# Performance work log

Hardware: AMD Instinct MI355X
Metric: run time of the kernel (lower is better)

Reference implementation:

```python
import jax, jax.numpy as jnp
import numpy as np

B, N_SPINS, D_MODEL, K_MC = 256, 128, 768, 25


def setup_inputs() -> dict:
    key = jax.random.key(0)
    k1, k2, k3 = jax.random.split(key, 3)
    features = jax.random.normal(k1, (B, N_SPINS, D_MODEL), dtype=jnp.float32)
    coalitions = jax.random.randint(k2, (K_MC, N_SPINS), 0, 2, dtype=jnp.int32)
    w_v = jax.random.normal(k3, (D_MODEL, D_MODEL), dtype=jnp.float32) * 0.02
    scale = jnp.full((1,), 0.1, dtype=jnp.float32)
    return {"features": features, "coalitions": coalitions, "w_v": w_v, "scale": scale}


def reference(features, coalitions, w_v, scale):
    # features: [B, n, d]; coalitions: [K, n] in {0,1}; w_v: [d, d]; scale: [1]
    c = coalitions.astype(features.dtype)                      # [K, n]
    # coalition_value batched over all K coalitions at once:
    # sum_j mask[k,j] * features[b,j,:]  (sum and linear proj commute)
    s = jnp.einsum('kn,bnd->bkd', c, features)                 # [B, K, d]
    proj = s @ w_v                                             # [B, K, d]
    norm = jnp.linalg.norm(proj, axis=-1)                      # [B, K]
    cv = jax.nn.relu(norm * scale[0])                          # coalition values [B, K]
    # Shapley estimate: mean(v | i in S) - mean(v | i not in S)
    cnt_with = c.sum(axis=0)                                   # [n]
    cnt_without = c.shape[0] - cnt_with
    v_with = (cv @ c) / jnp.maximum(cnt_with, 1.0)             # [B, n]
    v_without = (cv @ (1.0 - c)) / jnp.maximum(cnt_without, 1.0)
    valid = (cnt_with > 0) & (cnt_without > 0)                 # [n]
    shapley = jnp.where(valid, v_with - v_without, 0.0)        # [B, n]
    return shapley
```

## Files before the change

kernel.cpp:

```cpp
#include <hip/hip_runtime.h>
#include <hip/hip_bf16.h>
#include <stdint.h>

#define NB  256
#define NSP 128
#define DM  768
#define KMC 25
#define MROWS (NB*KMC)

#define OFF_S    0u
#define OFF_WT   9830400u
#define OFF_N2   11010048u
#define OFF_COEF 11035648u
#define OFF_CB   11049984u

typedef __attribute__((ext_vector_type(8))) short bf16x8;
typedef __attribute__((ext_vector_type(4))) float f32x4;
typedef unsigned int u32;

#define GLOAD_LDS16(gp, lp) \
  __builtin_amdgcn_global_load_lds((const __attribute__((address_space(1))) u32*)(gp), \
                                   (__attribute__((address_space(3))) u32*)(lp), 16, 0, 0)

__global__ __launch_bounds__(256) void prep_kernel(const float* __restrict__ wv,
                                                   const int* __restrict__ co,
                                                   char* __restrict__ ws) {
  const int blk = blockIdx.x;
  const int t = threadIdx.x;
  if (blk < 144) {
    __shared__ __hip_bfloat16 lt[64][66];
    const int bi = blk / 12, bj = blk % 12;
    const int k0 = bi * 64, n0 = bj * 64;
    #pragma unroll
    for (int i = 0; i < 16; ++i) {
      int idx = t + i * 256;
      int r = idx >> 6, c = idx & 63;
      lt[c][r] = __float2bfloat16(wv[(size_t)(k0 + r) * DM + n0 + c]);
    }
    __syncthreads();
    __hip_bfloat16* wT = (__hip_bfloat16*)(ws + OFF_WT);
    #pragma unroll
    for (int i = 0; i < 16; ++i) {
      int idx = t + i * 256;
      int r = idx >> 6, c = idx & 63;
      wT[(size_t)(n0 + r) * DM + k0 + c] = lt[r][c];
    }
  } else if (blk == 144) {
    if (t < NSP) {
      const int n = t;
      int cw = 0;
      for (int k = 0; k < KMC; ++k) cw += co[k * NSP + n];
      const int cwo = KMC - cw;
      const bool valid = (cw > 0) && (cwo > 0);
      float* coefT = (float*)(ws + OFF_COEF);
      for (int k = 0; k < 28; ++k) {
        float v = 0.f;
        if (valid && k < KMC) v = co[k * NSP + n] ? (1.f / (float)cw) : (-1.f / (float)cwo);
        coefT[n * 28 + k] = v;
      }
    }
  } else if (blk < 170) {
    int i = (blk - 145) * 256 + t;
    if (i < MROWS) ((float*)(ws + OFF_N2))[i] = 0.f;
  } else {
    __hip_bfloat16* Cb = (__hip_bfloat16*)(ws + OFF_CB);
    for (int i = t; i < 32 * NSP; i += 256) {
      int k = i >> 7, n = i & 127;
      float v = (k < KMC) ? (float)co[k * NSP + n] : 0.f;
      Cb[i] = __float2bfloat16(v);
    }
  }
}

__global__ __launch_bounds__(256) void kA(const float* __restrict__ f,
                                          const __hip_bfloat16* __restrict__ Cb,
                                          __hip_bfloat16* __restrict__ s) {
  const int b = blockIdx.x;
  const int half = blockIdx.y;
  const int tid = threadIdx.x;
  const int w = tid >> 6;
  const int lane = tid & 63;
  const int lo = lane & 15, hi = lane >> 4;

  bf16x8 A0[4], A1[4];
  #pragma unroll
  for (int ks = 0; ks < 4; ++ks) {
    A0[ks] = *(const bf16x8*)(Cb + (size_t)lo * NSP + ks * 32 + hi * 8);
    A1[ks] = *(const bf16x8*)(Cb + (size_t)(16 + lo) * NSP + ks * 32 + hi * 8);
  }

  const int dbase = half * 384 + w * 96;
  const float* fb = f + (size_t)b * NSP * DM + dbase + lo;

#define LOADT(dt, buf) { \
    const float* p_ = fb + (dt) * 16; \
    _Pragma("unroll") for (int ks = 0; ks < 4; ++ks) \
      _Pragma("unroll") for (int j = 0; j < 8; ++j) \
        buf[ks * 8 + j] = p_[(size_t)(ks * 32 + hi * 8 + j) * DM]; }

#define COMPUTE(dt, buf) { \
    bf16x8 Bf[4]; \
    _Pragma("unroll") for (int ks = 0; ks < 4; ++ks) \
      _Pragma("unroll") for (int j = 0; j < 8; ++j) { \
        __hip_bfloat16 h_ = __float2bfloat16(buf[ks * 8 + j]); \
        Bf[ks][j] = *(short*)&h_; } \
    f32x4 ac0 = {0.f, 0.f, 0.f, 0.f}, ac1 = {0.f, 0.f, 0.f, 0.f}; \
    _Pragma("unroll") for (int ks = 0; ks < 4; ++ks) { \
      ac0 = __builtin_amdgcn_mfma_f32_16x16x32_bf16(A0[ks], Bf[ks], ac0, 0, 0, 0); \
      ac1 = __builtin_amdgcn_mfma_f32_16x16x32_bf16(A1[ks], Bf[ks], ac1, 0, 0, 0); } \
    _Pragma("unroll") for (int i = 0; i < 4; ++i) { \
      int r0_ = hi * 4 + i; \
      s[((size_t)(b * KMC) + r0_) * DM + dbase + (dt) * 16 + lo] = __float2bfloat16(ac0[i]); \
      int r1_ = 16 + hi * 4 + i; \
      if (r1_ < KMC) \
        s[((size_t)(b * KMC) + r1_) * DM + dbase + (dt) * 16 + lo] = __float2bfloat16(ac1[i]); } }

  float bufA[32], bufB[32];
  LOADT(0, bufA)
  #pragma unroll
  for (int dt = 0; dt < 6; dt += 2) {
    if (dt + 1 < 6) LOADT(dt + 1, bufB)
    COMPUTE(dt, bufA)
    if (dt + 2 < 6) LOADT(dt + 2, bufA)
    if (dt + 1 < 6) COMPUTE(dt + 1, bufB)
  }
#undef LOADT
#undef COMPUTE
}

#define BM 128
#define BN 192
#define BK 32
#define NTK 24

__global__ __launch_bounds__(256) void kB(char* __restrict__ ws) {
  const int bid = blockIdx.x;
  const int tm = bid >> 2;
  const int tn = bid & 3;
  const int tid = threadIdx.x;
  const int wid = tid >> 6;
  const int lane = tid & 63;
  const int wm = wid >> 1;
  const int wn = wid & 1;

  const __hip_bfloat16* S  = (const __hip_bfloat16*)(ws + OFF_S);
  const __hip_bfloat16* WT = (const __hip_bfloat16*)(ws + OFF_WT);
  float* norm2 = (float*)(ws + OFF_N2);

  __shared__ __align__(16) char As[2][BM * BK * 2];
  __shared__ __align__(16) char Bs[2][BN * BK * 2];

  const char* gA[2]; char *lA0[2], *lA1[2];
  #pragma unroll
  for (int j = 0; j < 2; ++j) {
    int li = (wid * 2 + j) * 64 + lane;
    int r = li >> 2, sl = li & 3;
    int slx = sl ^ ((r >> 1) & 3);
    gA[j] = (const char*)(S + (size_t)(tm * BM + r) * DM) + slx * 16;
    lA0[j] = As[0] + (wid * 2 + j) * 1024;
    lA1[j] = As[1] + (wid * 2 + j) * 1024;
  }
  const char* gB[3]; char *lB0[3], *lB1[3];
  #pragma unroll
  for (int j = 0; j < 3; ++j) {
    int li = (wid * 3 + j) * 64 + lane;
    int r = li >> 2, sl = li & 3;
    int slx = sl ^ ((r >> 1) & 3);
    gB[j] = (const char*)(WT + (size_t)(tn * BN + r) * DM) + slx * 16;
    lB0[j] = Bs[0] + (wid * 3 + j) * 1024;
    lB1[j] = Bs[1] + (wid * 3 + j) * 1024;
  }

  auto stage = [&](int tk, int bsel) {
    size_t koff = (size_t)tk * (BK * 2);
    #pragma unroll
    for (int j = 0; j < 2; ++j) GLOAD_LDS16(gA[j] + koff, bsel ? lA1[j] : lA0[j]);
    #pragma unroll
    for (int j = 0; j < 3; ++j) GLOAD_LDS16(gB[j] + koff, bsel ? lB1[j] : lB0[j]);
  };

  f32x4 acc[4][6];
  #pragma unroll
  for (int m = 0; m < 4; ++m)
    #pragma unroll
    for (int n = 0; n < 6; ++n)
      #pragma unroll
      for (int j = 0; j < 4; ++j) acc[m][n][j] = 0.f;

  int offA[4], offB[6];
  #pragma unroll
  for (int m = 0; m < 4; ++m) {
    int r = wm * 64 + m * 16 + (lane & 15);
    int sl = (lane >> 4) ^ ((r >> 1) & 3);
    offA[m] = r * 64 + sl * 16;
  }
  #pragma unroll
  for (int n = 0; n < 6; ++n) {
    int r = wn * 96 + n * 16 + (lane & 15);
    int sl = (lane >> 4) ^ ((r >> 1) & 3);
    offB[n] = r * 64 + sl * 16;
  }

  stage(0, 0);
  for (int tk = 0; tk < NTK; ++tk) {
    int cur = tk & 1;
    __syncthreads();
    if (tk + 1 < NTK) stage(tk + 1, cur ^ 1);
    bf16x8 af[4], bfr[6];
    #pragma unroll
    for (int m = 0; m < 4; ++m) af[m] = *(const bf16x8*)(As[cur] + offA[m]);
    #pragma unroll
    for (int n = 0; n < 6; ++n) bfr[n] = *(const bf16x8*)(Bs[cur] + offB[n]);
    #pragma unroll
    for (int m = 0; m < 4; ++m)
      #pragma unroll
      for (int n = 0; n < 6; ++n)
        acc[m][n] = __builtin_amdgcn_mfma_f32_16x16x32_bf16(af[m], bfr[n], acc[m][n], 0, 0, 0);
  }

  float ps[4][4];
  #pragma unroll
  for (int m = 0; m < 4; ++m)
    #pragma unroll
    for (int i = 0; i < 4; ++i) {
      float v = 0.f;
      #pragma unroll
      for (int n = 0; n < 6; ++n) { float x = acc[m][n][i]; v += x * x; }
      #pragma unroll
      for (int d = 1; d < 16; d <<= 1) v += __shfl_xor(v, d, 64);
      ps[m][i] = v;
    }
  if ((lane & 15) == 0) {
    int g = lane >> 4;
    #pragma unroll
    for (int m = 0; m < 4; ++m)
      #pragma unroll
      for (int i = 0; i < 4; ++i)
        atomicAdd(&norm2[tm * BM + wm * 64 + m * 16 + g * 4 + i], ps[m][i]);
  }
}

__global__ __launch_bounds__(128) void kC(const char* __restrict__ ws,
                                          const float* __restrict__ scale,
                                          float* __restrict__ out) {
  const int b = blockIdx.x, n = threadIdx.x;
  const float* norm2 = (const float*)(ws + OFF_N2);
  const float* coefT = (const float*)(ws + OFF_COEF);
  __shared__ float cvs[32];
  if (n < KMC) {
    float nv = norm2[b * KMC + n];
    cvs[n] = fmaxf(sqrtf(fmaxf(nv, 0.f)) * scale[0], 0.f);
  } else if (n < 32) {
    cvs[n] = 0.f;
  }
  __syncthreads();
  float sum = 0.f;
  #pragma unroll
  for (int k = 0; k < KMC; ++k) sum += cvs[k] * coefT[n * 28 + k];
  out[b * NSP + n] = sum;
}

extern "C" void kernel_launch(void* const* d_in, const int* in_sizes, int n_in,
                              void* d_out, int out_size, void* d_ws, size_t ws_size,
                              hipStream_t stream) {
  const float* features   = (const float*)d_in[0];
  const int*   coalitions = (const int*)d_in[1];
  const float* wv         = (const float*)d_in[2];
  const float* scale      = (const float*)d_in[3];
  char* ws = (char*)d_ws;

  prep_kernel<<<171, 256, 0, stream>>>(wv, coalitions, ws);
  dim3 ga(NB, 2);
  kA<<<ga, 256, 0, stream>>>(features, (const __hip_bfloat16*)(ws + OFF_CB),
                             (__hip_bfloat16*)(ws + OFF_S));
  kB<<<200, 256, 0, stream>>>(ws);
  kC<<<NB, 128, 0, stream>>>(ws, scale, (float*)d_out);
}
```

Baseline: 52.52 us.

## Stage kA feature tiles through LDS with async global-to-LDS double buffering

Kernel kA now streams the feature slab into LDS using global_load_lds 16-byte transfers with a two-stage double buffer across the K steps, instead of strided per-thread scalar global loads into registers. The grid is split into four d-slices per batch instead of two, and launch bounds request 3 blocks per CU. The prep kernel also spreads the coalition-to-bf16 conversion across 32 blocks and unrolls the small loops. The aim is coalesced, wide feature reads and more parallelism, at the cost of 48KB of LDS per block and extra barriers.

Result: faster. 50.92 us (-3.1%).

```diff
diff --git a/kernel.cpp b/kernel.cpp
--- a/kernel.cpp
+++ b/kernel.cpp
@@ -49,10 +49,12 @@
     if (t < NSP) {
       const int n = t;
       int cw = 0;
+      #pragma unroll
       for (int k = 0; k < KMC; ++k) cw += co[k * NSP + n];
       const int cwo = KMC - cw;
       const bool valid = (cw > 0) && (cwo > 0);
       float* coefT = (float*)(ws + OFF_COEF);
+      #pragma unroll
       for (int k = 0; k < 28; ++k) {
         float v = 0.f;
         if (valid && k < KMC) v = co[k * NSP + n] ? (1.f / (float)cw) : (-1.f / (float)cwo);
@@ -63,25 +65,26 @@
     int i = (blk - 145) * 256 + t;
     if (i < MROWS) ((float*)(ws + OFF_N2))[i] = 0.f;
   } else {
-    __hip_bfloat16* Cb = (__hip_bfloat16*)(ws + OFF_CB);
-    for (int i = t; i < 32 * NSP; i += 256) {
-      int k = i >> 7, n = i & 127;
-      float v = (k < KMC) ? (float)co[k * NSP + n] : 0.f;
-      Cb[i] = __float2bfloat16(v);
-    }
-  }
-}
-
-__global__ __launch_bounds__(256) void kA(const float* __restrict__ f,
-                                          const __hip_bfloat16* __restrict__ Cb,
-                                          __hip_bfloat16* __restrict__ s) {
+    int k = blk - 170;
+    if (t < NSP) {
+      float v = (k < KMC) ? (float)co[k * NSP + t] : 0.f;
+      ((__hip_bfloat16*)(ws + OFF_CB))[k * NSP + t] = __float2bfloat16(v);
+    }
+  }
+}
+
+__global__ __launch_bounds__(256, 3) void kA(const float* __restrict__ f,
+                                             const __hip_bfloat16* __restrict__ Cb,
+                                             __hip_bfloat16* __restrict__ s) {
   const int b = blockIdx.x;
-  const int half = blockIdx.y;
+  const int dslice = blockIdx.y;
   const int tid = threadIdx.x;
   const int w = tid >> 6;
   const int lane = tid & 63;
   const int lo = lane & 15, hi = lane >> 4;
 
+  __shared__ __align__(16) float Fs[2][32 * 192];
+
   bf16x8 A0[4], A1[4];
   #pragma unroll
   for (int ks = 0; ks < 4; ++ks) {
@@ -89,43 +92,60 @@
     A1[ks] = *(const bf16x8*)(Cb + (size_t)(16 + lo) * NSP + ks * 32 + hi * 8);
   }
 
-  const int dbase = half * 384 + w * 96;
-  const float* fb = f + (size_t)b * NSP * DM + dbase + lo;
-
-#define LOADT(dt, buf) { \
-    const float* p_ = fb + (dt) * 16; \
-    _Pragma("unroll") for (int ks = 0; ks < 4; ++ks) \
-      _Pragma("unroll") for (int j = 0; j < 8; ++j) \
-        buf[ks * 8 + j] = p_[(size_t)(ks * 32 + hi * 8 + j) * DM]; }
-
-#define COMPUTE(dt, buf) { \
-    bf16x8 Bf[4]; \
-    _Pragma("unroll") for (int ks = 0; ks < 4; ++ks) \
-      _Pragma("unroll") for (int j = 0; j < 8; ++j) { \
-        __hip_bfloat16 h_ = __float2bfloat16(buf[ks * 8 + j]); \
-        Bf[ks][j] = *(short*)&h_; } \
-    f32x4 ac0 = {0.f, 0.f, 0.f, 0.f}, ac1 = {0.f, 0.f, 0.f, 0.f}; \
-    _Pragma("unroll") for (int ks = 0; ks < 4; ++ks) { \
-      ac0 = __builtin_amdgcn_mfma_f32_16x16x32_bf16(A0[ks], Bf[ks], ac0, 0, 0, 0); \
-      ac1 = __builtin_amdgcn_mfma_f32_16x16x32_bf16(A1[ks], Bf[ks], ac1, 0, 0, 0); } \
-    _Pragma("unroll") for (int i = 0; i < 4; ++i) { \
-      int r0_ = hi * 4 + i; \
-      s[((size_t)(b * KMC) + r0_) * DM + dbase + (dt) * 16 + lo] = __float2bfloat16(ac0[i]); \
-      int r1_ = 16 + hi * 4 + i; \
-      if (r1_ < KMC) \
-        s[((size_t)(b * KMC) + r1_) * DM + dbase + (dt) * 16 + lo] = __float2bfloat16(ac1[i]); } }
-
-  float bufA[32], bufB[32];
-  LOADT(0, bufA)
-  #pragma unroll
-  for (int dt = 0; dt < 6; dt += 2) {
-    if (dt + 1 < 6) LOADT(dt + 1, bufB)
-    COMPUTE(dt, bufA)
-    if (dt + 2 < 6) LOADT(dt + 2, bufA)
-    if (dt + 1 < 6) COMPUTE(dt + 1, bufB)
-  }
-#undef LOADT
-#undef COMPUTE
+  const float* fbase = f + (size_t)b * NSP * DM + dslice * 192;
+  const float* gsrc[6];
+  #pragma unroll
+  for (int q = 0; q < 6; ++q) {
+    int e = (w * 6 + q) * 256 + lane * 4;
+    int r = e / 192, c = e % 192;
+    gsrc[q] = fbase + (size_t)r * DM + c;
+  }
+
+  f32x4 ac0[3], ac1[3];
+  #pragma unroll
+  for (int ct = 0; ct < 3; ++ct)
+    #pragma unroll
+    for (int i = 0; i < 4; ++i) { ac0[ct][i] = 0.f; ac1[ct][i] = 0.f; }
+
+  #pragma unroll
+  for (int q = 0; q < 6; ++q)
+    GLOAD_LDS16(gsrc[q], &Fs[0][(w * 6 + q) * 256]);
+
+  #pragma unroll
+  for (int ks = 0; ks < 4; ++ks) {
+    const int bb = ks & 1;
+    __syncthreads();
+    if (ks < 3) {
+      #pragma unroll
+      for (int q = 0; q < 6; ++q)
+        GLOAD_LDS16(gsrc[q] + (size_t)(ks + 1) * 32 * DM, &Fs[bb ^ 1][(w * 6 + q) * 256]);
+    }
+    #pragma unroll
+    for (int ct = 0; ct < 3; ++ct) {
+      bf16x8 Bf;
+      #pragma unroll
+      for (int j = 0; j < 8; ++j) {
+        float v = Fs[bb][(hi * 8 + j) * 192 + w * 48 + ct * 16 + lo];
+        __hip_bfloat16 h = __float2bfloat16(v);
+        Bf[j] = *(short*)&h;
+      }
+      ac0[ct] = __builtin_amdgcn_mfma_f32_16x16x32_bf16(A0[ks], Bf, ac0[ct], 0, 0, 0);
+      ac1[ct] = __builtin_amdgcn_mfma_f32_16x16x32_bf16(A1[ks], Bf, ac1[ct], 0, 0, 0);
+    }
+  }
+
+  #pragma unroll
+  for (int ct = 0; ct < 3; ++ct) {
+    int dcol = dslice * 192 + w * 48 + ct * 16 + lo;
+    #pragma unroll
+    for (int i = 0; i < 4; ++i) {
+      int r0 = hi * 4 + i;
+      s[((size_t)b * KMC + r0) * DM + dcol] = __float2bfloat16(ac0[ct][i]);
+      int r1 = 16 + hi * 4 + i;
+      if (r1 < KMC)
+        s[((size_t)b * KMC + r1) * DM + dcol] = __float2bfloat16(ac1[ct][i]);
+    }
+  }
 }
 
 #define BM 128
@@ -269,8 +289,8 @@
   const float* scale      = (const float*)d_in[3];
   char* ws = (char*)d_ws;
 
-  prep_kernel<<<171, 256, 0, stream>>>(wv, coalitions, ws);
-  dim3 ga(NB, 2);
+  prep_kernel<<<202, 256, 0, stream>>>(wv, coalitions, ws);
+  dim3 ga(NB, 4);
   kA<<<ga, 256, 0, stream>>>(features, (const __hip_bfloat16*)(ws + OFF_CB),
                              (__hip_bfloat16*)(ws + OFF_S));
   kB<<<200, 256, 0, stream>>>(ws);
```
